# Kernel tuning notes

Measured on AMD Instinct MI355X. Metric: run time of the kernel, lower is better.

The kernel has to match this reference:

```python
import jax, jax.numpy as jnp
import numpy as np


def setup_inputs() -> dict:
    key = jax.random.key(0)
    x = jax.random.normal(key, (64, 256, 56, 56), dtype=jnp.float32)
    return {"x": x}


def reference(x):
    # Per-sample (over all dims except batch) min/max fake-quantization,
    # then dequantize, then hardtanh(0, 6) == ReLU6.
    B = x.shape[0]
    xf = x.reshape(B, -1)
    m = xf.min(axis=1).reshape((B,) + (1,) * (x.ndim - 1))  # per-sample min
    M = xf.max(axis=1).reshape((B,) + (1,) * (x.ndim - 1))  # per-sample max
    rng = M - m
    q = jnp.round(254.0 * (x - m) / rng - 127.0) / 1000.0
    y = (1000.0 * q + 127.0) * rng / 254.0 + m
    return jnp.clip(y, 0.0, 6.0)
```

## Files before the change

### kernel.cpp

```cpp
#include <hip/hip_runtime.h>
#include <math.h>


#define SAMPLE_V4    200704
#define NSAMPLES     64
#define BPS          49
#define V4_PER_BLK   4096

typedef __attribute__((ext_vector_type(4))) float fvec4;

__device__ __forceinline__ void acc_minmax(float4 v, float& mn, float& mx) {
    mn = fminf(mn, fminf(fminf(v.x, v.y), fminf(v.z, v.w)));
    mx = fmaxf(mx, fmaxf(fmaxf(v.x, v.y), fmaxf(v.z, v.w)));
}

__global__ __launch_bounds__(256) void qr_reduce(const float4* __restrict__ x,
                                                 float* __restrict__ pmin,
                                                 float* __restrict__ pmax) {
    const int s = blockIdx.x / BPS;
    const int b = blockIdx.x % BPS;
    const float4* base = x + (size_t)s * SAMPLE_V4 + (size_t)b * V4_PER_BLK;

    float mn0 = INFINITY, mx0 = -INFINITY, mn1 = INFINITY, mx1 = -INFINITY;
    float mn2 = INFINITY, mx2 = -INFINITY, mn3 = INFINITY, mx3 = -INFINITY;
    for (int i = threadIdx.x; i < V4_PER_BLK; i += 1024) {
        float4 v0 = base[i];
        float4 v1 = base[i + 256];
        float4 v2 = base[i + 512];
        float4 v3 = base[i + 768];
        acc_minmax(v0, mn0, mx0);
        acc_minmax(v1, mn1, mx1);
        acc_minmax(v2, mn2, mx2);
        acc_minmax(v3, mn3, mx3);
    }
    float mn = fminf(fminf(mn0, mn1), fminf(mn2, mn3));
    float mx = fmaxf(fmaxf(mx0, mx1), fmaxf(mx2, mx3));
    #pragma unroll
    for (int o = 32; o > 0; o >>= 1) {
        mn = fminf(mn, __shfl_down(mn, o, 64));
        mx = fmaxf(mx, __shfl_down(mx, o, 64));
    }
    __shared__ float smn[4], smx[4];
    const int wave = threadIdx.x >> 6;
    if ((threadIdx.x & 63) == 0) { smn[wave] = mn; smx[wave] = mx; }
    __syncthreads();
    if (threadIdx.x == 0) {
        pmin[blockIdx.x] = fminf(fminf(smn[0], smn[1]), fminf(smn[2], smn[3]));
        pmax[blockIdx.x] = fmaxf(fmaxf(smx[0], smx[1]), fmaxf(smx[2], smx[3]));
    }
}

__device__ __forceinline__ float qr_apply1(float x, float m, float sc, float inv) {
    float k = rintf((x - m) * inv - 127.0f);
    float y = fmaf(k + 127.0f, sc, m);
    return fminf(fmaxf(y, 0.0f), 6.0f);
}

__device__ __forceinline__ fvec4 qr_apply4(float4 v, float m, float sc, float inv) {
    fvec4 o;
    o.x = qr_apply1(v.x, m, sc, inv);
    o.y = qr_apply1(v.y, m, sc, inv);
    o.z = qr_apply1(v.z, m, sc, inv);
    o.w = qr_apply1(v.w, m, sc, inv);
    return o;
}

__global__ __launch_bounds__(256) void qr_apply(const float4* __restrict__ x,
                                                float4* __restrict__ y,
                                                const float* __restrict__ pmin,
                                                const float* __restrict__ pmax) {
    const int s = blockIdx.x / BPS;
    const int b = blockIdx.x % BPS;

    __shared__ float sp[3];
    if (threadIdx.x < 64) {
        float fmn = (threadIdx.x < BPS) ? pmin[s * BPS + threadIdx.x] : INFINITY;
        float fmx = (threadIdx.x < BPS) ? pmax[s * BPS + threadIdx.x] : -INFINITY;
        #pragma unroll
        for (int o = 32; o > 0; o >>= 1) {
            fmn = fminf(fmn, __shfl_down(fmn, o, 64));
            fmx = fmaxf(fmx, __shfl_down(fmx, o, 64));
        }
        if (threadIdx.x == 0) {
            const float rng = fmx - fmn;
            sp[0] = fmn;
            sp[1] = rng * (1.0f / 254.0f);
            sp[2] = 254.0f / rng;
        }
    }
    __syncthreads();
    const float m = sp[0], sc = sp[1], inv = sp[2];

    const size_t off = (size_t)s * SAMPLE_V4 + (size_t)b * V4_PER_BLK;
    const float4* xb = x + off;
    fvec4* yb = (fvec4*)(y + off);
    for (int i = threadIdx.x; i < V4_PER_BLK; i += 512) {
        float4 v0 = xb[i];
        float4 v1 = xb[i + 256];
        fvec4 o0 = qr_apply4(v0, m, sc, inv);
        fvec4 o1 = qr_apply4(v1, m, sc, inv);
        __builtin_nontemporal_store(o0, &yb[i]);
        __builtin_nontemporal_store(o1, &yb[i + 256]);
    }
}

extern "C" void kernel_launch(void* const* d_in, const int* in_sizes, int n_in,
                              void* d_out, int out_size, void* d_ws, size_t ws_size,
                              hipStream_t stream) {
    const float* x = (const float*)d_in[0];
    float* out = (float*)d_out;

    float* pmin = (float*)d_ws;
    float* pmax = pmin + NSAMPLES * BPS;

    qr_reduce<<<NSAMPLES * BPS, 256, 0, stream>>>((const float4*)x, pmin, pmax);
    qr_apply<<<NSAMPLES * BPS, 256, 0, stream>>>((const float4*)x, (float4*)out,
                                                 pmin, pmax);
}
```

Before: 368.7 us.

## Fuse min/max reduction and quantize apply into one pass with per-sample atomic barrier

Replaces the two-kernel reduce-then-apply scheme with a single kernel. Each block keeps its 16 float4 values per thread in registers, reduces a block min/max, and publishes it through order-preserving integer atomics into a per-sample slot. It then spins on a per-sample counter until all 49 blocks of that sample have arrived, and applies the quantization from registers. This removes the second global read of the input. In exchange it costs very high register pressure and low occupancy, and the cross-block spin wait relies on all blocks of a sample being co-resident; a guard counter bounds the wait.

```diff
diff --git a/kernel.cpp b/kernel.cpp
--- a/kernel.cpp
+++ b/kernel.cpp
@@ -2,51 +2,33 @@
 #include <math.h>
 
 
-#define SAMPLE_V4    200704
-#define NSAMPLES     64
-#define BPS          49
-#define V4_PER_BLK   4096
+#define SAMPLE_V4  200704
+#define NSAMPLES   64
+#define BPS        49
+#define V4_PER_BLK 4096
+#define LPT        16
 
 typedef __attribute__((ext_vector_type(4))) float fvec4;
 
-__device__ __forceinline__ void acc_minmax(float4 v, float& mn, float& mx) {
-    mn = fminf(mn, fminf(fminf(v.x, v.y), fminf(v.z, v.w)));
-    mx = fmaxf(mx, fmaxf(fmaxf(v.x, v.y), fmaxf(v.z, v.w)));
+struct __align__(128) Slot {
+    unsigned umin, umax, cnt;
+    unsigned pad[29];
+};
+
+__device__ __forceinline__ unsigned enc_f(float f) {
+    unsigned u = __float_as_uint(f);
+    return (u & 0x80000000u) ? ~u : (u | 0x80000000u);
+}
+__device__ __forceinline__ float dec_f(unsigned e) {
+    return __uint_as_float((e & 0x80000000u) ? (e ^ 0x80000000u) : ~e);
 }
 
-__global__ __launch_bounds__(256) void qr_reduce(const float4* __restrict__ x,
-                                                 float* __restrict__ pmin,
-                                                 float* __restrict__ pmax) {
-    const int s = blockIdx.x / BPS;
-    const int b = blockIdx.x % BPS;
-    const float4* base = x + (size_t)s * SAMPLE_V4 + (size_t)b * V4_PER_BLK;
-
-    float mn0 = INFINITY, mx0 = -INFINITY, mn1 = INFINITY, mx1 = -INFINITY;
-    float mn2 = INFINITY, mx2 = -INFINITY, mn3 = INFINITY, mx3 = -INFINITY;
-    for (int i = threadIdx.x; i < V4_PER_BLK; i += 1024) {
-        float4 v0 = base[i];
-        float4 v1 = base[i + 256];
-        float4 v2 = base[i + 512];
-        float4 v3 = base[i + 768];
-        acc_minmax(v0, mn0, mx0);
-        acc_minmax(v1, mn1, mx1);
-        acc_minmax(v2, mn2, mx2);
-        acc_minmax(v3, mn3, mx3);
-    }
-    float mn = fminf(fminf(mn0, mn1), fminf(mn2, mn3));
-    float mx = fmaxf(fmaxf(mx0, mx1), fmaxf(mx2, mx3));
-    #pragma unroll
-    for (int o = 32; o > 0; o >>= 1) {
-        mn = fminf(mn, __shfl_down(mn, o, 64));
-        mx = fmaxf(mx, __shfl_down(mx, o, 64));
-    }
-    __shared__ float smn[4], smx[4];
-    const int wave = threadIdx.x >> 6;
-    if ((threadIdx.x & 63) == 0) { smn[wave] = mn; smx[wave] = mx; }
-    __syncthreads();
-    if (threadIdx.x == 0) {
-        pmin[blockIdx.x] = fminf(fminf(smn[0], smn[1]), fminf(smn[2], smn[3]));
-        pmax[blockIdx.x] = fmaxf(fmaxf(smx[0], smx[1]), fmaxf(smx[2], smx[3]));
+__global__ __launch_bounds__(64) void qr_init(Slot* ws) {
+    int t = threadIdx.x;
+    if (t < NSAMPLES) {
+        ws[t].umin = 0xFFFFFFFFu;
+        ws[t].umax = 0u;
+        ws[t].cnt  = 0u;
     }
 }
 
@@ -56,51 +38,67 @@
     return fminf(fmaxf(y, 0.0f), 6.0f);
 }
 
-__device__ __forceinline__ fvec4 qr_apply4(float4 v, float m, float sc, float inv) {
-    fvec4 o;
-    o.x = qr_apply1(v.x, m, sc, inv);
-    o.y = qr_apply1(v.y, m, sc, inv);
-    o.z = qr_apply1(v.z, m, sc, inv);
-    o.w = qr_apply1(v.w, m, sc, inv);
-    return o;
-}
+__global__ __launch_bounds__(256) void qr_fused(const float4* __restrict__ x,
+                                                fvec4* __restrict__ y,
+                                                Slot* __restrict__ ws) {
+    const int s = blockIdx.x / BPS;
+    const int b = blockIdx.x - s * BPS;
+    const size_t off = (size_t)s * SAMPLE_V4 + (size_t)b * V4_PER_BLK;
+    const float4* xb = x + off;
 
-__global__ __launch_bounds__(256) void qr_apply(const float4* __restrict__ x,
-                                                float4* __restrict__ y,
-                                                const float* __restrict__ pmin,
-                                                const float* __restrict__ pmax) {
-    const int s = blockIdx.x / BPS;
-    const int b = blockIdx.x % BPS;
+    float4 v[LPT];
+    #pragma unroll
+    for (int i = 0; i < LPT; ++i) v[i] = xb[threadIdx.x + 256 * i];
 
+    float mn = INFINITY, mx = -INFINITY;
+    #pragma unroll
+    for (int i = 0; i < LPT; ++i) {
+        mn = fminf(mn, fminf(fminf(v[i].x, v[i].y), fminf(v[i].z, v[i].w)));
+        mx = fmaxf(mx, fmaxf(fmaxf(v[i].x, v[i].y), fmaxf(v[i].z, v[i].w)));
+    }
+    #pragma unroll
+    for (int o = 32; o > 0; o >>= 1) {
+        mn = fminf(mn, __shfl_down(mn, o, 64));
+        mx = fmaxf(mx, __shfl_down(mx, o, 64));
+    }
+
+    __shared__ float smn[4], smx[4];
     __shared__ float sp[3];
-    if (threadIdx.x < 64) {
-        float fmn = (threadIdx.x < BPS) ? pmin[s * BPS + threadIdx.x] : INFINITY;
-        float fmx = (threadIdx.x < BPS) ? pmax[s * BPS + threadIdx.x] : -INFINITY;
-        #pragma unroll
-        for (int o = 32; o > 0; o >>= 1) {
-            fmn = fminf(fmn, __shfl_down(fmn, o, 64));
-            fmx = fmaxf(fmx, __shfl_down(fmx, o, 64));
-        }
-        if (threadIdx.x == 0) {
-            const float rng = fmx - fmn;
-            sp[0] = fmn;
-            sp[1] = rng * (1.0f / 254.0f);
-            sp[2] = 254.0f / rng;
-        }
+    const int wave = threadIdx.x >> 6;
+    if ((threadIdx.x & 63) == 0) { smn[wave] = mn; smx[wave] = mx; }
+    __syncthreads();
+
+    if (threadIdx.x == 0) {
+        float bmn = fminf(fminf(smn[0], smn[1]), fminf(smn[2], smn[3]));
+        float bmx = fmaxf(fmaxf(smx[0], smx[1]), fmaxf(smx[2], smx[3]));
+        Slot* sl = ws + s;
+        atomicMin(&sl->umin, enc_f(bmn));
+        atomicMax(&sl->umax, enc_f(bmx));
+        __threadfence();
+        __hip_atomic_fetch_add(&sl->cnt, 1u, __ATOMIC_RELEASE, __HIP_MEMORY_SCOPE_AGENT);
+        int guard = 1 << 22;
+        while (__hip_atomic_load(&sl->cnt, __ATOMIC_ACQUIRE, __HIP_MEMORY_SCOPE_AGENT) < BPS
+               && --guard)
+            __builtin_amdgcn_s_sleep(4);
+        float fmn = dec_f(__hip_atomic_load(&sl->umin, __ATOMIC_RELAXED, __HIP_MEMORY_SCOPE_AGENT));
+        float fmx = dec_f(__hip_atomic_load(&sl->umax, __ATOMIC_RELAXED, __HIP_MEMORY_SCOPE_AGENT));
+        const float rng = fmx - fmn;
+        sp[0] = fmn;
+        sp[1] = rng * (1.0f / 254.0f);
+        sp[2] = 254.0f / rng;
     }
     __syncthreads();
     const float m = sp[0], sc = sp[1], inv = sp[2];
 
-    const size_t off = (size_t)s * SAMPLE_V4 + (size_t)b * V4_PER_BLK;
-    const float4* xb = x + off;
-    fvec4* yb = (fvec4*)(y + off);
-    for (int i = threadIdx.x; i < V4_PER_BLK; i += 512) {
-        float4 v0 = xb[i];
-        float4 v1 = xb[i + 256];
-        fvec4 o0 = qr_apply4(v0, m, sc, inv);
-        fvec4 o1 = qr_apply4(v1, m, sc, inv);
-        __builtin_nontemporal_store(o0, &yb[i]);
-        __builtin_nontemporal_store(o1, &yb[i + 256]);
+    fvec4* yb = y + off;
+    #pragma unroll
+    for (int i = 0; i < LPT; ++i) {
+        fvec4 o;
+        o.x = qr_apply1(v[i].x, m, sc, inv);
+        o.y = qr_apply1(v[i].y, m, sc, inv);
+        o.z = qr_apply1(v[i].z, m, sc, inv);
+        o.w = qr_apply1(v[i].w, m, sc, inv);
+        __builtin_nontemporal_store(o, &yb[threadIdx.x + 256 * i]);
     }
 }
 
@@ -108,12 +106,8 @@
                               void* d_out, int out_size, void* d_ws, size_t ws_size,
                               hipStream_t stream) {
     const float* x = (const float*)d_in[0];
-    float* out = (float*)d_out;
+    Slot* ws = (Slot*)d_ws;
 
-    float* pmin = (float*)d_ws;
-    float* pmax = pmin + NSAMPLES * BPS;
-
-    qr_reduce<<<NSAMPLES * BPS, 256, 0, stream>>>((const float4*)x, pmin, pmax);
-    qr_apply<<<NSAMPLES * BPS, 256, 0, stream>>>((const float4*)x, (float4*)out,
-                                                 pmin, pmax);
+    qr_init<<<1, 64, 0, stream>>>(ws);
+    qr_fused<<<NSAMPLES * BPS, 256, 0, stream>>>((const float4*)x, (fvec4*)d_out, ws);
 }
```

Measured after the change: 690.8 us. 87.4% more time.
